# Performance work log

Measured on AMD Instinct MI355X. Metric: run time of the kernel, lower is better.

## Reference

```python
import jax, jax.numpy as jnp
import numpy as np

B, T, C, H, E, K = 4, 2048, 512, 2048, 8, 2


def setup_inputs() -> dict:
    key = jax.random.key(0)
    ks = jax.random.split(key, 7)
    s_r = 1.0 / np.sqrt(C)
    s_h = 1.0 / np.sqrt(H)
    return {
        "x": jax.random.normal(ks[0], (B, T, C), dtype=jnp.float32),
        "Wr": jax.random.uniform(ks[1], (C, E), jnp.float32, -s_r, s_r),
        "br": jax.random.uniform(ks[2], (E,), jnp.float32, -s_r, s_r),
        "W1": jax.random.uniform(ks[3], (E, C, H), jnp.float32, -s_r, s_r),
        "b1": jax.random.uniform(ks[4], (E, H), jnp.float32, -s_r, s_r),
        "W2": jax.random.uniform(ks[5], (E, H, C), jnp.float32, -s_h, s_h),
        "b2": jax.random.uniform(ks[6], (E, C), jnp.float32, -s_h, s_h),
    }


def reference(x, Wr, br, W1, b1, W2, b2):
    # Router logits [B,T,E]
    logits = jnp.einsum("btc,ce->bte", x, Wr) + br
    topk_vals, topk_idx = jax.lax.top_k(logits, K)  # [B,T,K]
    scores = jax.nn.softmax(topk_vals, axis=-1)  # softmax over the K selected
    # Combine weights per expert: gate[b,t,e] = sum_k scores[b,t,k]*(idx==e)
    onehot = jax.nn.one_hot(topk_idx, E, dtype=x.dtype)  # [B,T,K,E]
    gate = jnp.einsum("btk,btke->bte", scores, onehot)  # [B,T,E]
    # Dense-masked expert MLPs (tokens not routed to e have gate==0)
    h = jax.nn.relu(jnp.einsum("btc,ech->bteh", x, W1) + b1)  # [B,T,E,H]
    y = jnp.einsum("bteh,ehc->btec", h, W2) + b2  # [B,T,E,C]
    out = jnp.einsum("btec,bte->btc", y, gate)  # weighted combine
    return logits, topk_idx, out
```

## Files before the change

### kernel.cpp

```cpp
#include <hip/hip_runtime.h>
#include <hip/hip_bf16.h>

#define NTOK 8192
#define NASN 16384
#define C_ 512
#define H_ 2048
#define E_ 8
#define NCH 128
#define CHTOK 64
#define MAXT 136

typedef __bf16 bf16x8 __attribute__((ext_vector_type(8)));
typedef float f32x4 __attribute__((ext_vector_type(4)));

#define WS_COUNTS 0
#define WS_BASE   4096
#define WS_OFFS   8192
#define WS_T1S    8448
#define WS_INFO   8704
#define WS_TOKL   (WS_INFO + NTOK*16)
#define WS_GATE   (WS_TOKL + NASN*4)
#define WS_SLOTS  (WS_GATE + NASN*4)
#define WS_XG     (WS_SLOTS + NTOK*8)
#define WS_W1B    (WS_XG + (size_t)NASN*C_*2)
#define WS_W2B    (WS_W1B + (size_t)E_*H_*C_*2)
#define WS_HS     (WS_W2B + (size_t)E_*H_*C_*2)
#define WS_YS     WS_XG

__device__ __forceinline__ unsigned int f2bf(float f) {
  __hip_bfloat16 h = __float2bfloat16(f);
  return (unsigned int)*(unsigned short*)&h;
}

__device__ __forceinline__ void g2l16(const unsigned short* g, unsigned short* l) {
  __builtin_amdgcn_global_load_lds(
      (const __attribute__((address_space(1))) unsigned int*)g,
      (__attribute__((address_space(3))) unsigned int*)l, 16, 0, 0);
}

__global__ __launch_bounds__(256) void k_router(
    const float* __restrict__ x, const float* __restrict__ Wr,
    const float* __restrict__ br, float* __restrict__ out_logits,
    float* __restrict__ out_idx, int4* __restrict__ info,
    int* __restrict__ counts)
{
  int t = blockIdx.x * 4 + (threadIdx.x >> 6);
  int lane = threadIdx.x & 63;
  const float4* xr = (const float4*)(x + (size_t)t * C_);
  float4 x0 = xr[lane*2], x1 = xr[lane*2+1];
  float xs[8] = {x0.x,x0.y,x0.z,x0.w,x1.x,x1.y,x1.z,x1.w};
  float acc[8] = {0,0,0,0,0,0,0,0};
  #pragma unroll
  for (int j = 0; j < 8; j++) {
    const float4* w = (const float4*)(Wr + (size_t)(lane*8+j) * E_);
    float4 w0 = w[0], w1 = w[1];
    float we[8] = {w0.x,w0.y,w0.z,w0.w,w1.x,w1.y,w1.z,w1.w};
    #pragma unroll
    for (int e = 0; e < 8; e++) acc[e] += xs[j] * we[e];
  }
  #pragma unroll
  for (int off = 1; off < 64; off <<= 1) {
    #pragma unroll
    for (int e = 0; e < 8; e++) acc[e] += __shfl_xor(acc[e], off, 64);
  }
  #pragma unroll
  for (int e = 0; e < 8; e++) acc[e] += br[e];
  if (lane == 0) {
    #pragma unroll
    for (int e = 0; e < 8; e++) out_logits[t*8 + e] = acc[e];
    int i0 = 0; float v0 = acc[0];
    #pragma unroll
    for (int e = 1; e < 8; e++) if (acc[e] > v0) { v0 = acc[e]; i0 = e; }
    int i1 = -1; float v1 = -1e30f;
    #pragma unroll
    for (int e = 0; e < 8; e++) if (e != i0 && acc[e] > v1) { v1 = acc[e]; i1 = e; }
    float d = expf(v1 - v0);
    float s1 = d / (1.0f + d);
    float s0 = 1.0f - s1;
    out_idx[t*2]     = (float)i0;
    out_idx[t*2 + 1] = (float)i1;
    info[t] = make_int4(i0, i1, __float_as_int(s0), __float_as_int(s1));
    int ch = t >> 6;
    atomicAdd(&counts[ch*8 + i0], 1);
    atomicAdd(&counts[ch*8 + i1], 1);
  }
}

__global__ __launch_bounds__(256) void k_prefix(
    const int* __restrict__ counts, int* __restrict__ base,
    int* __restrict__ offs, int* __restrict__ t1s)
{
  __shared__ int lc[NCH*8];
  __shared__ int tot[8];
  __shared__ int off_s[9];
  int tid = threadIdx.x;
  for (int i = tid; i < NCH*8; i += 256) lc[i] = counts[i];
  __syncthreads();
  if (tid < 8) {
    int run = 0;
    for (int c = 0; c < NCH; c++) { int v = lc[c*8+tid]; lc[c*8+tid] = run; run += v; }
    tot[tid] = run;
  }
  __syncthreads();
  if (tid == 0) {
    int o = 0, t = 0;
    off_s[0] = 0; offs[0] = 0; t1s[0] = 0;
    for (int e = 0; e < 8; e++) {
      o += tot[e];
      off_s[e+1] = o; offs[e+1] = o;
      t += (tot[e] + 127) >> 7;
      t1s[e+1] = t;
    }
  }
  __syncthreads();
  for (int i = tid; i < NCH*8; i += 256) base[i] = off_s[i & 7] + lc[i];
}

__global__ __launch_bounds__(64) void k_scatter(
    const int4* __restrict__ info, const int* __restrict__ base,
    int* __restrict__ tokl, float* __restrict__ gate, int2* __restrict__ slots2)
{
  __shared__ int cur[8];
  int c = blockIdx.x, tid = threadIdx.x;
  if (tid < 8) cur[tid] = base[c*8 + tid];
  __syncthreads();
  int t = c * CHTOK + tid;
  int4 nfo = info[t];
  int r0 = atomicAdd(&cur[nfo.x], 1);
  int r1 = atomicAdd(&cur[nfo.y], 1);
  tokl[r0] = t; gate[r0] = __int_as_float(nfo.z);
  tokl[r1] = t; gate[r1] = __int_as_float(nfo.w);
  slots2[t] = make_int2(r0, r1);
}

__global__ __launch_bounds__(256) void k_gather(
    const float* __restrict__ x, const int* __restrict__ tokl,
    unsigned short* __restrict__ Xg)
{
  int slot = blockIdx.x * 4 + (threadIdx.x >> 6);
  int lane = threadIdx.x & 63;
  int t = tokl[slot];
  const float4* xr = (const float4*)(x + (size_t)t * C_);
  float4 x0 = xr[lane*2], x1 = xr[lane*2+1];
  uint4 pk;
  pk.x = f2bf(x0.x) | (f2bf(x0.y) << 16);
  pk.y = f2bf(x0.z) | (f2bf(x0.w) << 16);
  pk.z = f2bf(x1.x) | (f2bf(x1.y) << 16);
  pk.w = f2bf(x1.z) | (f2bf(x1.w) << 16);
  *(uint4*)(Xg + (size_t)slot * C_ + lane*8) = pk;
}

__global__ __launch_bounds__(256) void k_transpose(
    const float* __restrict__ in, unsigned short* __restrict__ outp, int R, int S)
{
  __shared__ float tile[32][33];
  size_t zo = (size_t)blockIdx.z * R * S;
  in += zo; outp += zo;
  int s0 = blockIdx.x * 32, r0 = blockIdx.y * 32;
  int tx = threadIdx.x, ty = threadIdx.y;
  #pragma unroll
  for (int i = 0; i < 4; i++)
    tile[ty + i*8][tx] = in[(size_t)(r0 + ty + i*8) * S + s0 + tx];
  __syncthreads();
  #pragma unroll
  for (int i = 0; i < 4; i++)
    outp[(size_t)(s0 + ty + i*8) * R + r0 + tx] = f2bf(tile[tx][ty + i*8]);
}

__global__ __launch_bounds__(256) void k_gemm1(
    const unsigned short* __restrict__ Xg, const unsigned short* __restrict__ W1b,
    const float* __restrict__ b1, unsigned short* __restrict__ Hs,
    const int* __restrict__ offs, const int* __restrict__ t1s)
{
  __shared__ __align__(16) unsigned short AB[2*128*64];
  unsigned short* Al = AB;
  unsigned short* Bl = AB + 128*64;
  int mt = blockIdx.y;
  if (mt >= t1s[8]) return;
  int e = 0;
  #pragma unroll
  for (int i = 0; i < 7; i++) if (mt >= t1s[e+1]) e++;
  int row0 = offs[e] + (mt - t1s[e]) * 128;
  int rowEnd = offs[e+1];
  int n0 = blockIdx.x * 128;
  int tid = threadIdx.x, lane = tid & 63, w = tid >> 6;
  int wm = (w & 1) * 64, wn = (w >> 1) * 64;
  int quad = lane >> 4, l16 = lane & 15;
  const f32x4 zero = {0.f, 0.f, 0.f, 0.f};
  f32x4 acc[4][4];
  #pragma unroll
  for (int i = 0; i < 4; i++)
    #pragma unroll
    for (int j = 0; j < 4; j++) acc[i][j] = zero;
  const unsigned short* Bsrc = W1b + ((size_t)e * H_ + n0) * C_;

  const unsigned short* ga[4]; const unsigned short* gb[4];
  unsigned short* la[4]; unsigned short* lb[4];
  #pragma unroll
  for (int j = 0; j < 4; j++) {
    int L = (w*4 + j)*64 + lane;
    int row = L >> 3;
    int cc = (L & 7) ^ (row & 7);
    int gr = row0 + row; gr = gr < NASN-1 ? gr : NASN-1;
    ga[j] = Xg + (size_t)gr * C_ + cc*8;
    gb[j] = Bsrc + (size_t)row * C_ + cc*8;
    la[j] = Al + (w*4 + j)*512;
    lb[j] = Bl + (w*4 + j)*512;
  }
  int r7 = l16 & 7;

  for (int kk = 0; kk < C_; kk += 64) {
    #pragma unroll
    for (int j = 0; j < 4; j++) {
      g2l16(ga[j] + kk, la[j]);
      g2l16(gb[j] + kk, lb[j]);
    }
    __syncthreads();
    #pragma unroll
    for (int ks4 = 0; ks4 < 8; ks4 += 4) {
      int chunk = (ks4 + quad) ^ r7;
      bf16x8 af[4], bfr[4];
      #pragma unroll
      for (int i = 0; i < 4; i++)
        af[i] = *(const bf16x8*)&Al[(wm + i*16 + l16)*64 + chunk*8];
      #pragma unroll
      for (int j = 0; j < 4; j++)
        bfr[j] = *(const bf16x8*)&Bl[(wn + j*16 + l16)*64 + chunk*8];
      #pragma unroll
      for (int i = 0; i < 4; i++)
        #pragma unroll
        for (int j = 0; j < 4; j++)
          acc[i][j] = __builtin_amdgcn_mfma_f32_16x16x32_bf16(af[i], bfr[j], acc[i][j], 0, 0, 0);
    }
    __syncthreads();
  }

  unsigned short* Lt = AB + w*4096;
  #pragma unroll
  for (int j = 0; j < 4; j++) {
    int n = n0 + wn + j*16 + l16;
    float bias = b1[e * H_ + n];
    #pragma unroll
    for (int i = 0; i < 4; i++)
      #pragma unroll
      for (int r = 0; r < 4; r++) {
        float v = acc[i][j][r] + bias;
        Lt[(i*16 + quad*4 + r)*64 + j*16 + l16] = (unsigned short)f2bf(v > 0.f ? v : 0.f);
      }
  }
  #pragma unroll
  for (int it = 0; it < 8; it++) {
    int rloc = it*8 + (lane >> 3);
    int m = row0 + wm + rloc;
    uint4 vv = *(uint4*)&Lt[rloc*64 + (lane & 7)*8];
    if (m < rowEnd)
      *(uint4*)(Hs + (size_t)m * H_ + n0 + wn + (lane & 7)*8) = vv;
  }
}

__global__ __launch_bounds__(256) void k_gemm2(
    const unsigned short* __restrict__ Hs, const unsigned short* __restrict__ W2b,
    const float* __restrict__ b2, float* __restrict__ Ys,
    const int* __restrict__ offs, const int* __restrict__ t1s)
{
  __shared__ __align__(16) unsigned short AB[2*128*64];
  unsigned short* Al = AB;
  unsigned short* Bl = AB + 128*64;
  int mt = blockIdx.y;
  if (mt >= t1s[8]) return;
  int e = 0;
  #pragma unroll
  for (int i = 0; i < 7; i++) if (mt >= t1s[e+1]) e++;
  int row0 = offs[e] + (mt - t1s[e]) * 128;
  int rowEnd = offs[e+1];
  int n0 = blockIdx.x * 128;
  int tid = threadIdx.x, lane = tid & 63, w = tid >> 6;
  int wm = (w & 1) * 64, wn = (w >> 1) * 64;
  int quad = lane >> 4, l16 = lane & 15;
  const f32x4 zero = {0.f, 0.f, 0.f, 0.f};
  f32x4 acc[4][4];
  #pragma unroll
  for (int i = 0; i < 4; i++)
    #pragma unroll
    for (int j = 0; j < 4; j++) acc[i][j] = zero;
  const unsigned short* Bsrc = W2b + ((size_t)e * C_ + n0) * H_;

  const unsigned short* ga[4]; const unsigned short* gb[4];
  unsigned short* la[4]; unsigned short* lb[4];
  #pragma unroll
  for (int j = 0; j < 4; j++) {
    int L = (w*4 + j)*64 + lane;
    int row = L >> 3;
    int cc = (L & 7) ^ (row & 7);
    int gr = row0 + row; gr = gr < NASN-1 ? gr : NASN-1;
    ga[j] = Hs + (size_t)gr * H_ + cc*8;
    gb[j] = Bsrc + (size_t)row * H_ + cc*8;
    la[j] = Al + (w*4 + j)*512;
    lb[j] = Bl + (w*4 + j)*512;
  }
  int r7 = l16 & 7;

  for (int kk = 0; kk < H_; kk += 64) {
    #pragma unroll
    for (int j = 0; j < 4; j++) {
      g2l16(ga[j] + kk, la[j]);
      g2l16(gb[j] + kk, lb[j]);
    }
    __syncthreads();
    #pragma unroll
    for (int ks4 = 0; ks4 < 8; ks4 += 4) {
      int chunk = (ks4 + quad) ^ r7;
      bf16x8 af[4], bfr[4];
      #pragma unroll
      for (int i = 0; i < 4; i++)
        af[i] = *(const bf16x8*)&Al[(wm + i*16 + l16)*64 + chunk*8];
      #pragma unroll
      for (int j = 0; j < 4; j++)
        bfr[j] = *(const bf16x8*)&Bl[(wn + j*16 + l16)*64 + chunk*8];
      #pragma unroll
      for (int i = 0; i < 4; i++)
        #pragma unroll
        for (int j = 0; j < 4; j++)
          acc[i][j] = __builtin_amdgcn_mfma_f32_16x16x32_bf16(af[i], bfr[j], acc[i][j], 0, 0, 0);
    }
    __syncthreads();
  }

  float* Lt = (float*)AB + w*2048;
  #pragma unroll
  for (int h = 0; h < 2; h++) {
    #pragma unroll
    for (int j = 0; j < 4; j++) {
      int n = n0 + wn + j*16 + l16;
      float bias = b2[e * C_ + n];
      #pragma unroll
      for (int ii = 0; ii < 2; ii++) {
        int i = h*2 + ii;
        #pragma unroll
        for (int r = 0; r < 4; r++)
          Lt[(ii*16 + quad*4 + r)*64 + j*16 + l16] = acc[i][j][r] + bias;
      }
    }
    #pragma unroll
    for (int it = 0; it < 8; it++) {
      int rloc = it*4 + (lane >> 4);
      int m = row0 + wm + h*32 + rloc;
      float4 vv = *(float4*)&Lt[rloc*64 + (lane & 15)*4];
      if (m < rowEnd)
        *(float4*)(Ys + (size_t)m * C_ + n0 + wn + (lane & 15)*4) = vv;
    }
  }
}

__global__ __launch_bounds__(256) void k_combine(
    const float* __restrict__ Ys, const int4* __restrict__ info,
    const int2* __restrict__ slots2, float* __restrict__ outp)
{
  int t = blockIdx.x * 4 + (threadIdx.x >> 6);
  int lane = threadIdx.x & 63;
  int4 nfo = info[t];
  int2 ss = slots2[t];
  float g0 = __int_as_float(nfo.z), g1 = __int_as_float(nfo.w);
  const float4* ya = (const float4*)(Ys + (size_t)ss.x * C_);
  const float4* yb = (const float4*)(Ys + (size_t)ss.y * C_);
  float4* o = (float4*)(outp + (size_t)t * C_);
  #pragma unroll
  for (int i = 0; i < 2; i++) {
    float4 a = ya[lane*2 + i], b = yb[lane*2 + i];
    float4 r;
    r.x = g0*a.x + g1*b.x; r.y = g0*a.y + g1*b.y;
    r.z = g0*a.z + g1*b.z; r.w = g0*a.w + g1*b.w;
    o[lane*2 + i] = r;
  }
}

extern "C" void kernel_launch(void* const* d_in, const int* in_sizes, int n_in,
                              void* d_out, int out_size, void* d_ws, size_t ws_size,
                              hipStream_t stream)
{
  const float* x  = (const float*)d_in[0];
  const float* Wr = (const float*)d_in[1];
  const float* br = (const float*)d_in[2];
  const float* W1 = (const float*)d_in[3];
  const float* b1 = (const float*)d_in[4];
  const float* W2 = (const float*)d_in[5];
  const float* b2 = (const float*)d_in[6];
  float* out = (float*)d_out;
  char* ws = (char*)d_ws;

  int*  counts = (int*)(ws + WS_COUNTS);
  int*  base   = (int*)(ws + WS_BASE);
  int*  offs   = (int*)(ws + WS_OFFS);
  int*  t1s    = (int*)(ws + WS_T1S);
  int4* info   = (int4*)(ws + WS_INFO);
  int*  tokl   = (int*)(ws + WS_TOKL);
  float* gate  = (float*)(ws + WS_GATE);
  int2* slots2 = (int2*)(ws + WS_SLOTS);
  unsigned short* Xg  = (unsigned short*)(ws + WS_XG);
  unsigned short* W1b = (unsigned short*)(ws + WS_W1B);
  unsigned short* W2b = (unsigned short*)(ws + WS_W2B);
  unsigned short* Hs  = (unsigned short*)(ws + WS_HS);
  float* Ys = (float*)(ws + WS_YS);

  hipMemsetAsync(counts, 0, NCH*8*sizeof(int), stream);

  k_transpose<<<dim3(H_/32, C_/32, E_), dim3(32, 8), 0, stream>>>(W1, W1b, C_, H_);
  k_transpose<<<dim3(C_/32, H_/32, E_), dim3(32, 8), 0, stream>>>(W2, W2b, H_, C_);
  k_router<<<NTOK/4, 256, 0, stream>>>(x, Wr, br, out, out + 65536, info, counts);
  k_prefix<<<1, 256, 0, stream>>>(counts, base, offs, t1s);
  k_scatter<<<NCH, 64, 0, stream>>>(info, base, tokl, gate, slots2);
  k_gather<<<NASN/4, 256, 0, stream>>>(x, tokl, Xg);
  k_gemm1<<<dim3(16, MAXT), 256, 0, stream>>>(Xg, W1b, b1, Hs, offs, t1s);
  k_gemm2<<<dim3(4, MAXT), 256, 0, stream>>>(Hs, W2b, b2, Ys, offs, t1s);
  k_combine<<<NTOK/4, 256, 0, stream>>>(Ys, info, slots2, out + 81920);
}
```

Baseline: 303.2 us.

## Double-buffer LDS tiles in second expert GEMM to overlap loads with MFMA

Doubles the shared-memory tile buffer in the second GEMM and prefetches the next K-slice into the alternate buffer while the current one feeds MFMAs. Explicit vmcnt waits and raw barriers replace the two __syncthreads per iteration, so global-to-LDS latency can hide behind compute. LDS use per block doubles, which may reduce occupancy. Extra barriers are added around the epilogue staging.

```diff
diff --git a/kernel.cpp b/kernel.cpp
--- a/kernel.cpp
+++ b/kernel.cpp
@@ -263,9 +263,7 @@
     const float* __restrict__ b2, float* __restrict__ Ys,
     const int* __restrict__ offs, const int* __restrict__ t1s)
 {
-  __shared__ __align__(16) unsigned short AB[2*128*64];
-  unsigned short* Al = AB;
-  unsigned short* Bl = AB + 128*64;
+  __shared__ __align__(16) unsigned short AB[2*2*128*64];
   int mt = blockIdx.y;
   if (mt >= t1s[8]) return;
   int e = 0;
@@ -295,35 +293,51 @@
     int gr = row0 + row; gr = gr < NASN-1 ? gr : NASN-1;
     ga[j] = Hs + (size_t)gr * H_ + cc*8;
     gb[j] = Bsrc + (size_t)row * H_ + cc*8;
-    la[j] = Al + (w*4 + j)*512;
-    lb[j] = Bl + (w*4 + j)*512;
+    la[j] = AB + (w*4 + j)*512;
+    lb[j] = AB + 8192 + (w*4 + j)*512;
   }
   int r7 = l16 & 7;
-
-  for (int kk = 0; kk < H_; kk += 64) {
-    #pragma unroll
-    for (int j = 0; j < 4; j++) {
-      g2l16(ga[j] + kk, la[j]);
-      g2l16(gb[j] + kk, lb[j]);
-    }
-    __syncthreads();
+  const int KI = H_ / 64;
+
+  #pragma unroll
+  for (int j = 0; j < 4; j++) { g2l16(ga[j], la[j]); g2l16(gb[j], lb[j]); }
+
+  for (int ki = 0; ki < KI; ki++) {
+    int p = ki & 1;
+    if (ki + 1 < KI) {
+      int off = (ki + 1) * 64;
+      int bo = (p ^ 1) * 16384;
+      #pragma unroll
+      for (int j = 0; j < 4; j++) {
+        g2l16(ga[j] + off, la[j] + bo);
+        g2l16(gb[j] + off, lb[j] + bo);
+      }
+      asm volatile("s_waitcnt vmcnt(8)" ::: "memory");
+    } else {
+      asm volatile("s_waitcnt vmcnt(0)" ::: "memory");
+    }
+    asm volatile("s_barrier" ::: "memory");
+
+    const unsigned short* Ap = AB + p*16384;
+    const unsigned short* Bp = AB + p*16384 + 8192;
     #pragma unroll
     for (int ks4 = 0; ks4 < 8; ks4 += 4) {
       int chunk = (ks4 + quad) ^ r7;
       bf16x8 af[4], bfr[4];
       #pragma unroll
       for (int i = 0; i < 4; i++)
-        af[i] = *(const bf16x8*)&Al[(wm + i*16 + l16)*64 + chunk*8];
+        af[i] = *(const bf16x8*)&Ap[(wm + i*16 + l16)*64 + chunk*8];
       #pragma unroll
       for (int j = 0; j < 4; j++)
-        bfr[j] = *(const bf16x8*)&Bl[(wn + j*16 + l16)*64 + chunk*8];
+        bfr[j] = *(const bf16x8*)&Bp[(wn + j*16 + l16)*64 + chunk*8];
       #pragma unroll
       for (int i = 0; i < 4; i++)
         #pragma unroll
         for (int j = 0; j < 4; j++)
           acc[i][j] = __builtin_amdgcn_mfma_f32_16x16x32_bf16(af[i], bfr[j], acc[i][j], 0, 0, 0);
     }
-    __syncthreads();
+    asm volatile("s_waitcnt lgkmcnt(0)" ::: "memory");
+    asm volatile("s_barrier" ::: "memory");
   }
 
   float* Lt = (float*)AB + w*2048;
@@ -341,6 +355,7 @@
           Lt[(ii*16 + quad*4 + r)*64 + j*16 + l16] = acc[i][j][r] + bias;
       }
     }
+    __syncthreads();
     #pragma unroll
     for (int it = 0; it < 8; it++) {
       int rloc = it*4 + (lane >> 4);
@@ -349,6 +364,7 @@
       if (m < rowEnd)
         *(float4*)(Ys + (size_t)m * C_ + n0 + wn + (lane & 15)*4) = vv;
     }
+    __syncthreads();
   }
 }
 
```

After: 300.5 us. No clear change (-0.9%).
